# Kernel optimization log

Hardware: AMD Instinct MI355X
Metric: run time of the kernel (lower is better)

The kernel has to match this reference:

```python
import jax, jax.numpy as jnp
import numpy as np

# Constants matching the module's forward-time configuration
NUM_STAGES = 2
HIDDEN_LENGTH = (512, 1024)   # per-stage video token lengths; S = sum = 1536
ENC_LEN = 128                 # text/encoder token length per sample
B, H, D = 8, 16, 64           # batch (interleaved over stages), heads, head_dim
SEQLENS = (np.array([640, 480, 560, 400], np.int32),     # valid lens, stage 0 (Lc=640)
           np.array([1152, 864, 1008, 720], np.int32))   # valid lens, stage 1 (Lc=1152)


def _pack_indices(seqlens, lc):
    return np.concatenate([i * lc + np.arange(l) for i, l in enumerate(seqlens)]).astype(np.int32)


def setup_inputs() -> dict:
    key = jax.random.key(0)
    ks = jax.random.split(key, 6)
    S = sum(HIDDEN_LENGTH)
    inp = {
        'query':         jax.random.normal(ks[0], (B, S, H, D), jnp.float32),
        'key':           jax.random.normal(ks[1], (B, S, H, D), jnp.float32),
        'value':         jax.random.normal(ks[2], (B, S, H, D), jnp.float32),
        'encoder_query': jax.random.normal(ks[3], (B, ENC_LEN, H, D), jnp.float32),
        'encoder_key':   jax.random.normal(ks[4], (B, ENC_LEN, H, D), jnp.float32),
        'encoder_value': jax.random.normal(ks[5], (B, ENC_LEN, H, D), jnp.float32),
        'indices_0': jnp.asarray(_pack_indices(SEQLENS[0], ENC_LEN + HIDDEN_LENGTH[0])),
        'indices_1': jnp.asarray(_pack_indices(SEQLENS[1], ENC_LEN + HIDDEN_LENGTH[1])),
        'seqlens_0': jnp.asarray(SEQLENS[0]),
        'seqlens_1': jnp.asarray(SEQLENS[1]),
        'heads': 16,
        'scale': jnp.asarray(0.125, jnp.float32),  # 1/sqrt(D)
    }
    return inp


def reference(query, key, value, encoder_query, encoder_key, encoder_value,
              indices_0, indices_1, seqlens_0, seqlens_1, heads, scale):
    # Per stage: take the interleaved batch slice, prepend encoder tokens,
    # run non-causal varlen attention (padded + key-masked == flash_attn_varlen),
    # then gather the valid (packed) rows — faithful to index_first_axis packing.
    indices = (indices_0, indices_1)
    seqlens = (seqlens_0, seqlens_1)
    neg = jnp.finfo(query.dtype).min
    outs = []
    i_sum = 0
    for idx, L in enumerate(HIDDEN_LENGTH):
        q_s = jnp.concatenate([encoder_query[idx::NUM_STAGES], query[idx::NUM_STAGES, i_sum:i_sum + L]], axis=1)
        k_s = jnp.concatenate([encoder_key[idx::NUM_STAGES],   key[idx::NUM_STAGES,   i_sum:i_sum + L]], axis=1)
        v_s = jnp.concatenate([encoder_value[idx::NUM_STAGES], value[idx::NUM_STAGES, i_sum:i_sum + L]], axis=1)
        lc = q_s.shape[1]                                    # enc_len + L
        kmask = jnp.arange(lc)[None, :] < seqlens[idx][:, None]   # [b, lc] key validity
        scores = jnp.einsum('bqhd,bkhd->bhqk', q_s, k_s) * scale  # [b,h,lc,lc]
        scores = jnp.where(kmask[:, None, None, :], scores, neg)
        attn = jax.nn.softmax(scores, axis=-1)
        o = jnp.einsum('bhqk,bkhd->bqhd', attn, v_s)              # [b,lc,h,d]
        o_flat = o.reshape(-1, o.shape[2], o.shape[3])            # [(b*lc),h,d]
        outs.append(o_flat[indices[idx]])                          # pack valid rows
        i_sum += L
    return jnp.concatenate(outs, axis=0)  # [total_packed_tokens, H, D]
```

## Files before the change

kernel.cpp:

```cpp
#include <hip/hip_runtime.h>
#include <hip/hip_bf16.h>

typedef __attribute__((ext_vector_type(8))) __bf16 bf16x8;
typedef __attribute__((ext_vector_type(8))) short short8;
typedef __attribute__((ext_vector_type(4))) float f32x4;
typedef __attribute__((ext_vector_type(4))) unsigned int uint4v;
typedef __attribute__((ext_vector_type(2))) unsigned int uint2v;

#define KS 72
#define LOG2E 1.44269504088896340736f

__device__ __forceinline__ unsigned pack2bf(float lo, float hi) {
    unsigned a = __builtin_bit_cast(unsigned, lo) + 0x8000u;
    unsigned b = __builtin_bit_cast(unsigned, hi) + 0x8000u;
    return __builtin_amdgcn_perm(b, a, 0x07060302u);
}

__device__ __forceinline__ bf16x8 ldfrag(const short* p) {
    short8 s = *reinterpret_cast<const short8*>(p);
    return __builtin_bit_cast(bf16x8, s);
}

__global__ __launch_bounds__(512, 6) void vfa_kernel(
    const float* __restrict__ qv, const float* __restrict__ kv, const float* __restrict__ vv,
    const float* __restrict__ eq, const float* __restrict__ ek, const float* __restrict__ ev,
    const float* __restrict__ scale_p, float* __restrict__ out)
{
    constexpr int H = 16, Dh = 64, ENC = 128, SV = 1536;
    constexpr int SS_CUM[9] = {0,144,272,384,480,560,640,704,768};
    constexpr int SEQL[8] = {1152,1008,864,720,640,560,480,400};
    constexpr int QTN[8]  = {9,8,7,6,5,5,4,4};
    constexpr int OB[8]   = {2080,4096,3232,5104,0,1120,640,1680};
    constexpr int BB[8]   = {1,5,3,7,0,4,2,6};
    constexpr int ISUM[8] = {512,512,512,512,0,0,0,0};

    __shared__ __align__(16) short smem[4*64*KS];

    const int bid = (blockIdx.x % 3) * 256 + (blockIdx.x / 3);
    int ss = 0;
    #pragma unroll
    for (int i = 1; i < 8; ++i) ss += (bid >= SS_CUM[i]) ? 1 : 0;
    const int seqlen   = SEQL[ss];
    const int nqt      = QTN[ss];
    const int b        = BB[ss];
    const int isum     = ISUM[ss];
    const int out_base = OB[ss];
    const int local    = bid - SS_CUM[ss];
    const int head     = local / nqt;
    const int qt       = local - head * nqt;

    const int tid  = threadIdx.x;
    const int wave = tid >> 6;
    const int lane = tid & 63;
    const int quad = lane >> 4;
    const int l15  = lane & 15;

    const float qmul = scale_p[0] * LOG2E;

    const int qrow = qt*128 + wave*16 + l15;
    const float* qrp;
    if (qrow < ENC) qrp = eq + ((b*ENC + qrow)*H + head)*Dh;
    else            qrp = qv + (((b*SV + isum) + (qrow - ENC))*H + head)*Dh;
    bf16x8 qfrag[2];
    #pragma unroll
    for (int f = 0; f < 2; ++f) {
        const float* p = qrp + f*32 + quad*8;
        f32x4 a = *reinterpret_cast<const f32x4*>(p);
        f32x4 c = *reinterpret_cast<const f32x4*>(p + 4);
        uint4v u;
        u[0] = pack2bf(a[0]*qmul, a[1]*qmul);
        u[1] = pack2bf(a[2]*qmul, a[3]*qmul);
        u[2] = pack2bf(c[0]*qmul, c[1]*qmul);
        u[3] = pack2bf(c[2]*qmul, c[3]*qmul);
        qfrag[f] = __builtin_bit_cast(bf16x8, u);
    }

    f32x4 acc[4];
    #pragma unroll
    for (int dt = 0; dt < 4; ++dt) acc[dt] = {0.f,0.f,0.f,0.f};
    float m_s = -INFINITY, l_s = 0.f;

    const int t2  = tid & 255;
    const int klk = t2 >> 2;
    const int kd  = (t2 & 3) * 16;
    const int vk0 = (t2 & 15) * 4;
    const int vd0 = (t2 >> 4) * 4;
    const bool krole = (tid < 256);
    const int klkp = (klk & 0x23) | ((klk & 0x04) << 2) | ((klk & 0x18) >> 1);

    f32x4 ld0, ld1, ld2, ld3;

    auto issue_loads = [&](int kt_) {
        if (krole) {
            const int kr = kt_*64 + klk;
            const float* krow;
            if (kr < ENC) krow = ek + ((b*ENC + kr)*H + head)*Dh;
            else          krow = kv + (((b*SV + isum) + (kr - ENC))*H + head)*Dh;
            ld0 = *reinterpret_cast<const f32x4*>(krow + kd);
            ld1 = *reinterpret_cast<const f32x4*>(krow + kd + 4);
            ld2 = *reinterpret_cast<const f32x4*>(krow + kd + 8);
            ld3 = *reinterpret_cast<const f32x4*>(krow + kd + 12);
        } else {
            #pragma unroll
            for (int i = 0; i < 4; ++i) {
                const int kr = kt_*64 + vk0 + i;
                const float* vrow;
                if (kr < ENC) vrow = ev + ((b*ENC + kr)*H + head)*Dh;
                else          vrow = vv + (((b*SV + isum) + (kr - ENC))*H + head)*Dh;
                f32x4 t = *reinterpret_cast<const f32x4*>(vrow + vd0);
                if (i == 0) ld0 = t; else if (i == 1) ld1 = t;
                else if (i == 2) ld2 = t; else ld3 = t;
            }
        }
    };

    auto write_tile = [&](short* kb, short* vb) {
        if (krole) {
            uint4v kp;
            kp[0] = pack2bf(ld0[0], ld0[1]);
            kp[1] = pack2bf(ld0[2], ld0[3]);
            kp[2] = pack2bf(ld1[0], ld1[1]);
            kp[3] = pack2bf(ld1[2], ld1[3]);
            *reinterpret_cast<uint4v*>(&kb[klkp*KS + kd]) = kp;
            kp[0] = pack2bf(ld2[0], ld2[1]);
            kp[1] = pack2bf(ld2[2], ld2[3]);
            kp[2] = pack2bf(ld3[0], ld3[1]);
            kp[3] = pack2bf(ld3[2], ld3[3]);
            *reinterpret_cast<uint4v*>(&kb[klkp*KS + kd + 8]) = kp;
        } else {
            #pragma unroll
            for (int j = 0; j < 4; ++j) {
                uint2v w;
                w[0] = pack2bf(ld0[j], ld1[j]);
                w[1] = pack2bf(ld2[j], ld3[j]);
                *reinterpret_cast<uint2v*>(&vb[(vd0 + j)*KS + vk0]) = w;
            }
        }
    };

    const int nkt = (seqlen + 63) >> 6;

    issue_loads(0);

    for (int kt = 0; kt < nkt; ++kt) {
        short* kb = smem + (kt & 1) * (2*64*KS);
        short* vb = kb + 64*KS;

        write_tile(kb, vb);
        if (kt + 1 < nkt) issue_loads(kt + 1);

        asm volatile("s_waitcnt lgkmcnt(0)" ::: "memory");
        __builtin_amdgcn_s_barrier();
        __builtin_amdgcn_sched_barrier(0);

        const int rem = seqlen - kt*64;

        float s[4][4];
        #pragma unroll
        for (int sub = 0; sub < 4; ++sub) {
            if (32*(sub >> 1) < rem) {
                const short* kr0 = &kb[(sub*16 + l15)*KS + quad*8];
                f32x4 sv = {0.f,0.f,0.f,0.f};
                sv = __builtin_amdgcn_mfma_f32_16x16x32_bf16(ldfrag(kr0),      qfrag[0], sv, 0,0,0);
                sv = __builtin_amdgcn_mfma_f32_16x16x32_bf16(ldfrag(kr0 + 32), qfrag[1], sv, 0,0,0);
                #pragma unroll
                for (int r = 0; r < 4; ++r) s[sub][r] = sv[r];
            } else {
                #pragma unroll
                for (int r = 0; r < 4; ++r) s[sub][r] = -INFINITY;
            }
        }
        if (rem < 64) {
            #pragma unroll
            for (int sub = 0; sub < 4; ++sub) {
                const bool vq = (32*(sub >> 1) + 8*quad + 4*(sub & 1)) < rem;
                #pragma unroll
                for (int r = 0; r < 4; ++r) s[sub][r] = vq ? s[sub][r] : -INFINITY;
            }
        }

        float mx = s[0][0];
        #pragma unroll
        for (int sub = 0; sub < 4; ++sub)
            #pragma unroll
            for (int r = 0; r < 4; ++r) mx = fmaxf(mx, s[sub][r]);
        mx = fmaxf(mx, __shfl_xor(mx, 16, 64));
        mx = fmaxf(mx, __shfl_xor(mx, 32, 64));
        const float mn = fmaxf(m_s, mx);
        const float alpha = __builtin_amdgcn_exp2f(m_s - mn);
        m_s = mn;
        #pragma unroll
        for (int dt = 0; dt < 4; ++dt)
            #pragma unroll
            for (int r = 0; r < 4; ++r) acc[dt][r] *= alpha;

        float rs = 0.f;
        unsigned pk[4][2];
        #pragma unroll
        for (int sub = 0; sub < 4; ++sub) {
            float p0 = __builtin_amdgcn_exp2f(s[sub][0] - mn);
            float p1 = __builtin_amdgcn_exp2f(s[sub][1] - mn);
            float p2 = __builtin_amdgcn_exp2f(s[sub][2] - mn);
            float p3 = __builtin_amdgcn_exp2f(s[sub][3] - mn);
            rs += (p0 + p1) + (p2 + p3);
            pk[sub][0] = pack2bf(p0, p1);
            pk[sub][1] = pack2bf(p2, p3);
        }
        rs += __shfl_xor(rs, 16, 64);
        rs += __shfl_xor(rs, 32, 64);
        l_s = l_s * alpha + rs;

        #pragma unroll
        for (int kstep = 0; kstep < 2; ++kstep) {
            if (32*kstep < rem) {
                uint4v pf;
                pf[0] = pk[kstep*2 + 0][0];
                pf[1] = pk[kstep*2 + 0][1];
                pf[2] = pk[kstep*2 + 1][0];
                pf[3] = pk[kstep*2 + 1][1];
                bf16x8 pfr = __builtin_bit_cast(bf16x8, pf);
                #pragma unroll
                for (int dt = 0; dt < 4; ++dt) {
                    bf16x8 vfr = ldfrag(&vb[(dt*16 + l15)*KS + kstep*32 + quad*8]);
                    acc[dt] = __builtin_amdgcn_mfma_f32_16x16x32_bf16(vfr, pfr, acc[dt], 0,0,0);
                }
            }
        }
    }

    __syncthreads();
    float* tbuf = reinterpret_cast<float*>(smem);
    const float inv = 1.0f / l_s;
    const int rowl = tid >> 3;
    const int colb = (tid & 7) * 8;
    #pragma unroll
    for (int p = 0; p < 2; ++p) {
        if (p) __syncthreads();
        if ((wave >> 2) == p) {
            #pragma unroll
            for (int dt = 0; dt < 4; ++dt) {
                f32x4 t = acc[dt] * inv;
                *reinterpret_cast<f32x4*>(&tbuf[((wave & 3)*16 + l15)*68 + dt*16 + quad*4]) = t;
            }
        }
        __syncthreads();
        const int grow = qt*128 + p*64 + rowl;
        if (grow < seqlen) {
            float* orow = out + (size_t)(out_base + grow)*(H*Dh) + head*Dh + colb;
            const float* trow = tbuf + rowl*68 + colb;
            *reinterpret_cast<float4*>(orow)     = *reinterpret_cast<const float4*>(trow);
            *reinterpret_cast<float4*>(orow + 4) = *reinterpret_cast<const float4*>(trow + 4);
        }
    }
}

extern "C" void kernel_launch(void* const* d_in, const int* in_sizes, int n_in,
                              void* d_out, int out_size, void* d_ws, size_t ws_size,
                              hipStream_t stream) {
    const float* q     = (const float*)d_in[0];
    const float* k     = (const float*)d_in[1];
    const float* v     = (const float*)d_in[2];
    const float* eq    = (const float*)d_in[3];
    const float* ek    = (const float*)d_in[4];
    const float* ev    = (const float*)d_in[5];
    const float* scale = (const float*)d_in[11];
    float* out = (float*)d_out;

    vfa_kernel<<<dim3(768), dim3(512), 0, stream>>>(q, k, v, eq, ek, ev, scale, out);
}
```

Baseline: 205.8 us.

## Process two 16-row query groups per wave to double K/V tile reuse

Each wave now holds two 16-row query fragments, so a block covers 256 query rows instead of 128. Every K/V tile staged in shared memory is therefore reused by twice as many queries, and the grid drops from 768 to 416 blocks with a new block-order mapping. The online softmax also skips the accumulator rescale unless the running max grows by more than 8, and waves whose rows lie entirely past the sequence end skip compute. In exchange each thread needs more registers (occupancy hint lowered from 6 to 4) and there are fewer blocks to fill the CUs.

```diff
diff --git a/kernel.cpp b/kernel.cpp
--- a/kernel.cpp
+++ b/kernel.cpp
@@ -21,22 +21,32 @@
     return __builtin_bit_cast(bf16x8, s);
 }
 
-__global__ __launch_bounds__(512, 6) void vfa_kernel(
+__global__ __launch_bounds__(512, 4) void vfa_kernel(
     const float* __restrict__ qv, const float* __restrict__ kv, const float* __restrict__ vv,
     const float* __restrict__ eq, const float* __restrict__ ek, const float* __restrict__ ev,
     const float* __restrict__ scale_p, float* __restrict__ out)
 {
     constexpr int H = 16, Dh = 64, ENC = 128, SV = 1536;
-    constexpr int SS_CUM[9] = {0,144,272,384,480,560,640,704,768};
+    constexpr int SS_CUM[9] = {0,80,144,208,256,304,352,384,416};
     constexpr int SEQL[8] = {1152,1008,864,720,640,560,480,400};
-    constexpr int QTN[8]  = {9,8,7,6,5,5,4,4};
+    constexpr int QTN[8]  = {5,4,4,3,3,3,2,2};
     constexpr int OB[8]   = {2080,4096,3232,5104,0,1120,640,1680};
     constexpr int BB[8]   = {1,5,3,7,0,4,2,6};
     constexpr int ISUM[8] = {512,512,512,512,0,0,0,0};
+    constexpr int LCM1[8] = {1151,1151,1151,1151,639,639,639,639};
 
     __shared__ __align__(16) short smem[4*64*KS];
 
-    const int bid = (blockIdx.x % 3) * 256 + (blockIdx.x / 3);
+    const int x = blockIdx.x;
+    int bid;
+    if (x < 160)      bid = 80 + x;
+    else if (x < 240) bid = x - 160;
+    else if (x < 256) bid = x;
+    else if (x < 288) bid = 128 + x;
+    else if (x < 320) bid = 64 + x;
+    else if (x < 368) bid = x - 16;
+    else              bid = x - 112;
+
     int ss = 0;
     #pragma unroll
     for (int i = 1; i < 8; ++i) ss += (bid >= SS_CUM[i]) ? 1 : 0;
@@ -57,28 +67,39 @@
 
     const float qmul = scale_p[0] * LOG2E;
 
-    const int qrow = qt*128 + wave*16 + l15;
-    const float* qrp;
-    if (qrow < ENC) qrp = eq + ((b*ENC + qrow)*H + head)*Dh;
-    else            qrp = qv + (((b*SV + isum) + (qrow - ENC))*H + head)*Dh;
-    bf16x8 qfrag[2];
+    bf16x8 qfrag[2][2];
     #pragma unroll
-    for (int f = 0; f < 2; ++f) {
-        const float* p = qrp + f*32 + quad*8;
-        f32x4 a = *reinterpret_cast<const f32x4*>(p);
-        f32x4 c = *reinterpret_cast<const f32x4*>(p + 4);
-        uint4v u;
-        u[0] = pack2bf(a[0]*qmul, a[1]*qmul);
-        u[1] = pack2bf(a[2]*qmul, a[3]*qmul);
-        u[2] = pack2bf(c[0]*qmul, c[1]*qmul);
-        u[3] = pack2bf(c[2]*qmul, c[3]*qmul);
-        qfrag[f] = __builtin_bit_cast(bf16x8, u);
+    for (int g = 0; g < 2; ++g) {
+        int qrow = qt*256 + wave*32 + g*16 + l15;
+        qrow = (qrow < LCM1[ss]) ? qrow : LCM1[ss];
+        const float* qrp;
+        if (qrow < ENC) qrp = eq + ((b*ENC + qrow)*H + head)*Dh;
+        else            qrp = qv + (((b*SV + isum) + (qrow - ENC))*H + head)*Dh;
+        #pragma unroll
+        for (int f = 0; f < 2; ++f) {
+            const float* p = qrp + f*32 + quad*8;
+            f32x4 a = *reinterpret_cast<const f32x4*>(p);
+            f32x4 c = *reinterpret_cast<const f32x4*>(p + 4);
+            uint4v u;
+            u[0] = pack2bf(a[0]*qmul, a[1]*qmul);
+            u[1] = pack2bf(a[2]*qmul, a[3]*qmul);
+            u[2] = pack2bf(c[0]*qmul, c[1]*qmul);
+            u[3] = pack2bf(c[2]*qmul, c[3]*qmul);
+            qfrag[g][f] = __builtin_bit_cast(bf16x8, u);
+        }
     }
 
-    f32x4 acc[4];
+    f32x4 acc[2][4];
     #pragma unroll
-    for (int dt = 0; dt < 4; ++dt) acc[dt] = {0.f,0.f,0.f,0.f};
-    float m_s = -INFINITY, l_s = 0.f;
+    for (int g = 0; g < 2; ++g)
+        #pragma unroll
+        for (int dt = 0; dt < 4; ++dt) acc[g][dt] = {0.f,0.f,0.f,0.f};
+    float m_s[2] = {-INFINITY, -INFINITY};
+    float l_s[2] = {0.f, 0.f};
+
+    const int qb   = qt*256 + wave*32;
+    const bool act0 = qb < seqlen;
+    const bool act1 = qb + 16 < seqlen;
 
     const int t2  = tid & 255;
     const int klk = t2 >> 2;
@@ -138,6 +159,41 @@
         }
     };
 
+    auto softmax_g = [&](const float (&s)[4][4], unsigned (&pk)[4][2],
+                         float &msg, float &lsg, f32x4 (&ac)[4]) {
+        float mx = s[0][0];
+        #pragma unroll
+        for (int sub = 0; sub < 4; ++sub)
+            #pragma unroll
+            for (int r = 0; r < 4; ++r) mx = fmaxf(mx, s[sub][r]);
+        mx = fmaxf(mx, __shfl_xor(mx, 16, 64));
+        mx = fmaxf(mx, __shfl_xor(mx, 32, 64));
+        if (__ballot(mx > msg + 8.f)) {
+            const float mn = fmaxf(msg, mx);
+            const float alpha = __builtin_amdgcn_exp2f(msg - mn);
+            msg = mn;
+            #pragma unroll
+            for (int dt = 0; dt < 4; ++dt)
+                #pragma unroll
+                for (int r = 0; r < 4; ++r) ac[dt][r] *= alpha;
+            lsg *= alpha;
+        }
+        float rs = 0.f;
+        #pragma unroll
+        for (int sub = 0; sub < 4; ++sub) {
+            float p0 = __builtin_amdgcn_exp2f(s[sub][0] - msg);
+            float p1 = __builtin_amdgcn_exp2f(s[sub][1] - msg);
+            float p2 = __builtin_amdgcn_exp2f(s[sub][2] - msg);
+            float p3 = __builtin_amdgcn_exp2f(s[sub][3] - msg);
+            rs += (p0 + p1) + (p2 + p3);
+            pk[sub][0] = pack2bf(p0, p1);
+            pk[sub][1] = pack2bf(p2, p3);
+        }
+        rs += __shfl_xor(rs, 16, 64);
+        rs += __shfl_xor(rs, 32, 64);
+        lsg += rs;
+    };
+
     const int nkt = (seqlen + 63) >> 6;
 
     issue_loads(0);
@@ -153,21 +209,28 @@
         __builtin_amdgcn_s_barrier();
         __builtin_amdgcn_sched_barrier(0);
 
+        if (!act0) continue;
+
         const int rem = seqlen - kt*64;
 
-        float s[4][4];
+        float s0[4][4], s1[4][4];
         #pragma unroll
         for (int sub = 0; sub < 4; ++sub) {
             if (32*(sub >> 1) < rem) {
                 const short* kr0 = &kb[(sub*16 + l15)*KS + quad*8];
+                bf16x8 kf0 = ldfrag(kr0);
+                bf16x8 kf1 = ldfrag(kr0 + 32);
                 f32x4 sv = {0.f,0.f,0.f,0.f};
-                sv = __builtin_amdgcn_mfma_f32_16x16x32_bf16(ldfrag(kr0),      qfrag[0], sv, 0,0,0);
-                sv = __builtin_amdgcn_mfma_f32_16x16x32_bf16(ldfrag(kr0 + 32), qfrag[1], sv, 0,0,0);
-                #pragma unroll
-                for (int r = 0; r < 4; ++r) s[sub][r] = sv[r];
+                sv = __builtin_amdgcn_mfma_f32_16x16x32_bf16(kf0, qfrag[0][0], sv, 0,0,0);
+                sv = __builtin_amdgcn_mfma_f32_16x16x32_bf16(kf1, qfrag[0][1], sv, 0,0,0);
+                f32x4 sw = {0.f,0.f,0.f,0.f};
+                sw = __builtin_amdgcn_mfma_f32_16x16x32_bf16(kf0, qfrag[1][0], sw, 0,0,0);
+                sw = __builtin_amdgcn_mfma_f32_16x16x32_bf16(kf1, qfrag[1][1], sw, 0,0,0);
+                #pragma unroll
+                for (int r = 0; r < 4; ++r) { s0[sub][r] = sv[r]; s1[sub][r] = sw[r]; }
             } else {
                 #pragma unroll
-                for (int r = 0; r < 4; ++r) s[sub][r] = -INFINITY;
+                for (int r = 0; r < 4; ++r) { s0[sub][r] = -INFINITY; s1[sub][r] = -INFINITY; }
             }
         }
         if (rem < 64) {
@@ -175,54 +238,38 @@
             for (int sub = 0; sub < 4; ++sub) {
                 const bool vq = (32*(sub >> 1) + 8*quad + 4*(sub & 1)) < rem;
                 #pragma unroll
-                for (int r = 0; r < 4; ++r) s[sub][r] = vq ? s[sub][r] : -INFINITY;
-            }
-        }
-
-        float mx = s[0][0];
-        #pragma unroll
-        for (int sub = 0; sub < 4; ++sub)
-            #pragma unroll
-            for (int r = 0; r < 4; ++r) mx = fmaxf(mx, s[sub][r]);
-        mx = fmaxf(mx, __shfl_xor(mx, 16, 64));
-        mx = fmaxf(mx, __shfl_xor(mx, 32, 64));
-        const float mn = fmaxf(m_s, mx);
-        const float alpha = __builtin_amdgcn_exp2f(m_s - mn);
-        m_s = mn;
-        #pragma unroll
-        for (int dt = 0; dt < 4; ++dt)
-            #pragma unroll
-            for (int r = 0; r < 4; ++r) acc[dt][r] *= alpha;
-
-        float rs = 0.f;
-        unsigned pk[4][2];
-        #pragma unroll
-        for (int sub = 0; sub < 4; ++sub) {
-            float p0 = __builtin_amdgcn_exp2f(s[sub][0] - mn);
-            float p1 = __builtin_amdgcn_exp2f(s[sub][1] - mn);
-            float p2 = __builtin_amdgcn_exp2f(s[sub][2] - mn);
-            float p3 = __builtin_amdgcn_exp2f(s[sub][3] - mn);
-            rs += (p0 + p1) + (p2 + p3);
-            pk[sub][0] = pack2bf(p0, p1);
-            pk[sub][1] = pack2bf(p2, p3);
-        }
-        rs += __shfl_xor(rs, 16, 64);
-        rs += __shfl_xor(rs, 32, 64);
-        l_s = l_s * alpha + rs;
+                for (int r = 0; r < 4; ++r) {
+                    s0[sub][r] = vq ? s0[sub][r] : -INFINITY;
+                    s1[sub][r] = vq ? s1[sub][r] : -INFINITY;
+                }
+            }
+        }
+
+        unsigned pk0[4][2], pk1[4][2];
+        softmax_g(s0, pk0, m_s[0], l_s[0], acc[0]);
+        if (act1) softmax_g(s1, pk1, m_s[1], l_s[1], acc[1]);
 
         #pragma unroll
         for (int kstep = 0; kstep < 2; ++kstep) {
             if (32*kstep < rem) {
                 uint4v pf;
-                pf[0] = pk[kstep*2 + 0][0];
-                pf[1] = pk[kstep*2 + 0][1];
-                pf[2] = pk[kstep*2 + 1][0];
-                pf[3] = pk[kstep*2 + 1][1];
-                bf16x8 pfr = __builtin_bit_cast(bf16x8, pf);
+                pf[0] = pk0[kstep*2 + 0][0];
+                pf[1] = pk0[kstep*2 + 0][1];
+                pf[2] = pk0[kstep*2 + 1][0];
+                pf[3] = pk0[kstep*2 + 1][1];
+                bf16x8 pfr0 = __builtin_bit_cast(bf16x8, pf);
+                uint4v pg;
+                pg[0] = pk1[kstep*2 + 0][0];
+                pg[1] = pk1[kstep*2 + 0][1];
+                pg[2] = pk1[kstep*2 + 1][0];
+                pg[3] = pk1[kstep*2 + 1][1];
+                bf16x8 pfr1 = __builtin_bit_cast(bf16x8, pg);
                 #pragma unroll
                 for (int dt = 0; dt < 4; ++dt) {
                     bf16x8 vfr = ldfrag(&vb[(dt*16 + l15)*KS + kstep*32 + quad*8]);
-                    acc[dt] = __builtin_amdgcn_mfma_f32_16x16x32_bf16(vfr, pfr, acc[dt], 0,0,0);
+                    acc[0][dt] = __builtin_amdgcn_mfma_f32_16x16x32_bf16(vfr, pfr0, acc[0][dt], 0,0,0);
+                    if (act1)
+                        acc[1][dt] = __builtin_amdgcn_mfma_f32_16x16x32_bf16(vfr, pfr1, acc[1][dt], 0,0,0);
                 }
             }
         }
@@ -230,21 +277,25 @@
 
     __syncthreads();
     float* tbuf = reinterpret_cast<float*>(smem);
-    const float inv = 1.0f / l_s;
+    const float inv0 = 1.0f / l_s[0];
+    const float inv1 = 1.0f / l_s[1];
     const int rowl = tid >> 3;
     const int colb = (tid & 7) * 8;
     #pragma unroll
-    for (int p = 0; p < 2; ++p) {
+    for (int p = 0; p < 4; ++p) {
         if (p) __syncthreads();
-        if ((wave >> 2) == p) {
+        if ((wave >> 1) == p) {
+            const int rb = (wave & 1) * 32;
             #pragma unroll
             for (int dt = 0; dt < 4; ++dt) {
-                f32x4 t = acc[dt] * inv;
-                *reinterpret_cast<f32x4*>(&tbuf[((wave & 3)*16 + l15)*68 + dt*16 + quad*4]) = t;
+                f32x4 tA = acc[0][dt] * inv0;
+                f32x4 tB = acc[1][dt] * inv1;
+                *reinterpret_cast<f32x4*>(&tbuf[(rb + l15)*68      + dt*16 + quad*4]) = tA;
+                *reinterpret_cast<f32x4*>(&tbuf[(rb + 16 + l15)*68 + dt*16 + quad*4]) = tB;
             }
         }
         __syncthreads();
-        const int grow = qt*128 + p*64 + rowl;
+        const int grow = qt*256 + p*64 + rowl;
         if (grow < seqlen) {
             float* orow = out + (size_t)(out_base + grow)*(H*Dh) + head*Dh + colb;
             const float* trow = tbuf + rowl*68 + colb;
@@ -266,5 +317,5 @@
     const float* scale = (const float*)d_in[11];
     float* out = (float*)d_out;
 
-    vfa_kernel<<<dim3(768), dim3(512), 0, stream>>>(q, k, v, eq, ek, ev, scale, out);
+    vfa_kernel<<<dim3(416), dim3(512), 0, stream>>>(q, k, v, eq, ek, ev, scale, out);
 }
```

After: 211.7 us. 2.9% more time.
